# Kernel optimization log

Hardware: AMD Instinct MI355X
Metric: run time of the kernel (lower is better)

Reference implementation:

```python
import jax, jax.numpy as jnp
import numpy as np

N = 50000   # nodes
E = 800000  # directed edges (self loops added in reference)
F = 8       # temporal features
D = 64      # hidden_channels
H = 4       # heads
C = D // H  # per-head channels = 16
L = 3       # num GAT layers
T = 3       # node types
TE = 16     # type embed dim


def _glorot(key, shape):
    fan_in, fan_out = shape[-2], shape[-1]
    s = jnp.sqrt(6.0 / (fan_in + fan_out))
    return jax.random.uniform(key, shape, jnp.float32, -s, s)


def setup_inputs() -> dict:
    key = jax.random.key(0)
    ks = jax.random.split(key, 24)
    return {
        'x': jax.random.normal(ks[0], (N, F), jnp.float32),
        'node_type': jax.random.randint(ks[1], (N,), 0, T),
        'edge_src': jax.random.randint(ks[2], (E,), 0, N),
        'edge_dst': jax.random.randint(ks[3], (E,), 0, N),
        # TemporalEncoder (Linear F->D + ReLU)
        'Wt': _glorot(ks[4], (F, D)), 'bt': jnp.zeros((D,), jnp.float32),
        # type embedding and input projection
        'Et': 0.1 * jax.random.normal(ks[5], (T, TE), jnp.float32),
        'Wp': _glorot(ks[6], (D + TE, D)), 'bp': jnp.zeros((D,), jnp.float32),
        # GATv2 layers (stacked over L)
        'Wl': _glorot(ks[7], (L, D, H * C)), 'bl': jnp.zeros((L, H * C), jnp.float32),
        'Wr': _glorot(ks[8], (L, D, H * C)), 'br': jnp.zeros((L, H * C), jnp.float32),
        'att': _glorot(ks[9], (L, H, C)),
        'Wres': _glorot(ks[10], (L, D, H * C)),
        'bconv': jnp.zeros((L, H * C), jnp.float32),
        'gamma': jnp.ones((L, D), jnp.float32), 'beta': jnp.zeros((L, D), jnp.float32),
        'alpha': jnp.float32(0.5),
        # output head
        'W1': _glorot(ks[11], (D, D // 2)), 'b1': jnp.zeros((D // 2,), jnp.float32),
        'W2': _glorot(ks[12], (D // 2, 1)), 'b2': jnp.zeros((1,), jnp.float32),
    }


def _layernorm(x, g, b, eps=1e-5):
    mu = jnp.mean(x, -1, keepdims=True)
    v = jnp.mean((x - mu) ** 2, -1, keepdims=True)
    return g * (x - mu) / jnp.sqrt(v + eps) + b


def reference(x, node_type, edge_src, edge_dst, Wt, bt, Et, Wp, bp,
              Wl, bl, Wr, br, att, Wres, bconv, gamma, beta, alpha,
              W1, b1, W2, b2):
    # temporal encoder + type embedding + input projection
    h = jax.nn.relu(x @ Wt + bt)                       # [N, D]
    h = jnp.concatenate([h, Et[node_type]], axis=-1) @ Wp + bp
    h0 = h

    # add self loops once (eval mode -> no dropout)
    loop = jnp.arange(N)
    src = jnp.concatenate([edge_src, loop])            # [E']
    dst = jnp.concatenate([edge_dst, loop])

    for l in range(L):
        xl = (h @ Wl[l] + bl[l]).reshape(N, H, C)      # source transform
        xr = (h @ Wr[l] + br[l]).reshape(N, H, C)      # target transform
        e = jax.nn.leaky_relu(xl[src] + xr[dst], 0.2)  # [E', H, C]
        score = jnp.einsum('ehc,hc->eh', e, att[l])    # [E', H]
        # segment softmax over incoming edges of each destination node
        m = jax.ops.segment_max(score, dst, num_segments=N)
        ex = jnp.exp(score - m[dst])
        s = jax.ops.segment_sum(ex, dst, num_segments=N)
        a = ex / (s[dst] + 1e-16)                      # [E', H]
        msg = xl[src] * a[:, :, None]                  # [E', H, C]
        out = jax.ops.segment_sum(msg, dst, num_segments=N).reshape(N, H * C)
        out = out + h @ Wres[l] + bconv[l]             # GATv2 residual + bias
        h = _layernorm(alpha * out + (1.0 - alpha) * h0, gamma[l], beta[l])

    z = jax.nn.relu(h @ W1 + b1)
    return jax.nn.sigmoid(z @ W2 + b2)                 # [N, 1]
```

## Files before the change

### kernel.cpp

```cpp
#include <hip/hip_runtime.h>
#include <hip/hip_bf16.h>

typedef __hip_bfloat16 bf16;
typedef __attribute__((ext_vector_type(8))) short short8;
typedef __attribute__((ext_vector_type(4))) float f32x4;

__device__ __forceinline__ float b2f(bf16 v) { return __bfloat162float(v); }
__device__ __forceinline__ bf16 f2b(float v) { return __float2bfloat16(v); }
__device__ __forceinline__ short f2bs(float v) {
    bf16 b = f2b(v);
    return *reinterpret_cast<short*>(&b);
}
__device__ __forceinline__ float bflo(unsigned int u) { return __uint_as_float(u << 16); }
__device__ __forceinline__ float bfhi(unsigned int u) { return __uint_as_float(u & 0xffff0000u); }
__device__ __forceinline__ unsigned int packbf(float lo, float hi) {
    bf16 l = f2b(lo), h = f2b(hi);
    return ((unsigned int)(*(unsigned short*)&h) << 16) | (*(unsigned short*)&l);
}


__global__ void k_sentinel(float* out, int n, float val) {
    int i = blockIdx.x * blockDim.x + threadIdx.x;
    if (i < n) out[i] = val;
}

#define PREP_BLOCKS 169
__global__ void k_setup(const float* __restrict__ Wl, const float* __restrict__ Wr,
                        const float* __restrict__ Wres, const float* __restrict__ Wp,
                        const float* __restrict__ W1, const float* __restrict__ Et,
                        const float* __restrict__ bp,
                        bf16* __restrict__ WT, bf16* __restrict__ WpT,
                        bf16* __restrict__ W1T, float* __restrict__ TyB,
                        const int* __restrict__ edst, int* __restrict__ counts,
                        int* __restrict__ rank, int e) {
    int b = blockIdx.x;
    if (b < PREP_BLOCKS) {
        int i = b * 256 + threadIdx.x;
        if (i < 36864) {
            int l = i / 12288, rem = i % 12288;
            int col = rem / 64, k = rem % 64;
            int mat = col >> 6, c = col & 63;
            const float* W = (mat == 0) ? Wl : (mat == 1) ? Wr : Wres;
            WT[i] = f2b(W[l * 4096 + k * 64 + c]);
        } else if (i < 40960) {
            int j = i - 36864, col = j / 64, k = j % 64;
            WpT[j] = f2b(Wp[k * 64 + col]);
        } else if (i < 43008) {
            int j = i - 40960, col = j / 64, k = j % 64;
            W1T[j] = f2b(W1[k * 32 + col]);
        } else if (i < 43200) {
            int j = i - 43008, t = j / 64, d = j % 64;
            float s = bp[d];
#pragma unroll
            for (int f = 0; f < 16; ++f) s += Et[t * 16 + f] * Wp[(64 + f) * 64 + d];
            TyB[j] = s;
        }
    } else {
        int i = (b - PREP_BLOCKS) * 256 + threadIdx.x;
        if (i < e) rank[i] = atomicAdd(&counts[edst[i]], 1);
    }
}

__global__ __launch_bounds__(256) void k_encx(
        const float* __restrict__ x, const int* __restrict__ ntype,
        const float* __restrict__ Wt, const float* __restrict__ bt,
        const bf16* __restrict__ WpT, const float* __restrict__ TyB,
        bf16* __restrict__ h0b,
        const bf16* __restrict__ WT0, const float* __restrict__ bl0,
        const float* __restrict__ br0, const float* __restrict__ bc0,
        bf16* __restrict__ xlo, bf16* __restrict__ xro, bf16* __restrict__ reso,
        int n) {
    __shared__ float sWt[512];
    __shared__ float sbt[64];
    __shared__ __align__(16) short sh[4 * 16 * 72];
    int tid = threadIdx.x;
    for (int i = tid; i < 512; i += 256) sWt[i] = Wt[i];
    if (tid < 64) sbt[tid] = bt[tid];
    __syncthreads();
    int wave = tid >> 6, lane = tid & 63;
    int nb = blockIdx.x * 64 + wave * 16;
    if (nb >= n) return;
    int m = lane & 15, q = lane >> 4;
    short* shw = sh + wave * 16 * 72;

    const float* xrow = x + (size_t)(nb + m) * 8;
    float xv[8];
#pragma unroll
    for (int f = 0; f < 8; ++f) xv[f] = xrow[f];

    short8 a0, a1;
#pragma unroll
    for (int j = 0; j < 8; ++j) {
        int c0 = q * 8 + j, c1 = 32 + q * 8 + j;
        float s0 = sbt[c0], s1 = sbt[c1];
#pragma unroll
        for (int f = 0; f < 8; ++f) {
            s0 += xv[f] * sWt[f * 64 + c0];
            s1 += xv[f] * sWt[f * 64 + c1];
        }
        a0[j] = f2bs(fmaxf(s0, 0.f));
        a1[j] = f2bs(fmaxf(s1, 0.f));
    }

    int ty[4];
#pragma unroll
    for (int r = 0; r < 4; ++r) ty[r] = ntype[nb + q * 4 + r];

#pragma unroll
    for (int t = 0; t < 4; ++t) {
        const short* wp = (const short*)(WpT + (size_t)(t * 16 + m) * 64) + q * 8;
        short8 b0 = *(const short8*)(wp);
        short8 b1 = *(const short8*)(wp + 32);
        f32x4 acc = {0.f, 0.f, 0.f, 0.f};
        acc = __builtin_amdgcn_mfma_f32_16x16x32_bf16(a0, b0, acc, 0, 0, 0);
        acc = __builtin_amdgcn_mfma_f32_16x16x32_bf16(a1, b1, acc, 0, 0, 0);
        int col = t * 16 + m;
#pragma unroll
        for (int r = 0; r < 4; ++r) {
            int nd = nb + q * 4 + r;
            short vb = f2bs(acc[r] + TyB[ty[r] * 64 + col]);
            h0b[(size_t)nd * 64 + col] = *reinterpret_cast<bf16*>(&vb);
            shw[(q * 4 + r) * 72 + col] = vb;
        }
    }
    short8 ha0 = *(const short8*)(&shw[m * 72 + q * 8]);
    short8 ha1 = *(const short8*)(&shw[m * 72 + 32 + q * 8]);
#pragma unroll
    for (int t = 0; t < 12; ++t) {
        const short* wp = (const short*)(WT0 + (size_t)(t * 16 + m) * 64) + q * 8;
        short8 b0 = *(const short8*)(wp);
        short8 b1 = *(const short8*)(wp + 32);
        f32x4 acc = {0.f, 0.f, 0.f, 0.f};
        acc = __builtin_amdgcn_mfma_f32_16x16x32_bf16(ha0, b0, acc, 0, 0, 0);
        acc = __builtin_amdgcn_mfma_f32_16x16x32_bf16(ha1, b1, acc, 0, 0, 0);
        int col = t * 16 + m;
        int mat = col >> 6, c = col & 63;
        float bias = (mat == 0) ? bl0[c] : (mat == 1) ? br0[c] : bc0[c];
        bf16* dst = (mat == 0) ? xlo : (mat == 1) ? xro : reso;
#pragma unroll
        for (int r = 0; r < 4; ++r)
            dst[(size_t)(nb + q * 4 + r) * 64 + c] = f2b(acc[r] + bias);
    }
}

__global__ void k_scan_local(const int* __restrict__ counts, int* __restrict__ row_raw,
                             int* __restrict__ bsum, int n) {
    __shared__ int part[256];
    int tid = threadIdx.x;
    int base = blockIdx.x * 1024 + tid * 4;
    int c0 = (base     < n) ? counts[base]     + 1 : 0;
    int c1 = (base + 1 < n) ? counts[base + 1] + 1 : 0;
    int c2 = (base + 2 < n) ? counts[base + 2] + 1 : 0;
    int c3 = (base + 3 < n) ? counts[base + 3] + 1 : 0;
    part[tid] = c0 + c1 + c2 + c3;
    __syncthreads();
    for (int off = 1; off < 256; off <<= 1) {
        int t = (tid >= off) ? part[tid - off] : 0;
        __syncthreads();
        part[tid] += t;
        __syncthreads();
    }
    int ex = (tid == 0) ? 0 : part[tid - 1];
    if (base     < n) row_raw[base]     = ex;
    if (base + 1 < n) row_raw[base + 1] = ex + c0;
    if (base + 2 < n) row_raw[base + 2] = ex + c0 + c1;
    if (base + 3 < n) row_raw[base + 3] = ex + c0 + c1 + c2;
    if (tid == 255) bsum[blockIdx.x] = part[255];
}

__global__ void k_scan_bsum(int* __restrict__ bsum, int* __restrict__ row_ptr,
                            int g, int n) {
    int lane = threadIdx.x;
    int orig = (lane < g) ? bsum[lane] : 0;
    int v = orig;
#pragma unroll
    for (int off = 1; off < 64; off <<= 1) {
        int t = __shfl_up(v, off, 64);
        if (lane >= off) v += t;
    }
    if (lane < g) bsum[lane] = v - orig;
    if (lane == 63) row_ptr[n] = v;
}

__global__ void k_build(const int* __restrict__ src, const int* __restrict__ dst,
                        const int* __restrict__ row_raw, const int* __restrict__ bsum,
                        const int* __restrict__ rank,
                        int* __restrict__ row_ptr, int* __restrict__ csr_src,
                        int n, int e) {
    int i = blockIdx.x * 256 + threadIdx.x;
    if (i < n) {
        int rp = row_raw[i] + bsum[i >> 10];
        row_ptr[i] = rp;
        csr_src[rp] = i;
    }
    if (i < e) {
        int d = dst[i];
        int pos = row_raw[d] + bsum[d >> 10] + 1 + rank[i];
        csr_src[pos] = src[i];
    }
}

#define GAT2_STEP(E_IDX, LS, A0S, A1S)                                            \
    {                                                                             \
        int s_ = csr_src[E_IDX];                                                  \
        unsigned int xu_ = *(const unsigned int*)((const unsigned short*)xl +     \
                                                  (size_t)s_ * 64 + ch);          \
        float x0_ = bflo(xu_), x1_ = bfhi(xu_);                                   \
        float t0_ = x0_ + xr0; t0_ = fmaxf(t0_, 0.2f * t0_);                      \
        float t1_ = x1_ + xr1; t1_ = fmaxf(t1_, 0.2f * t1_);                      \
        float p_ = t0_ * at0 + t1_ * at1;                                         \
        p_ += __shfl_xor(p_, 1, 64);                                              \
        p_ += __shfl_xor(p_, 2, 64);                                              \
        p_ += __shfl_xor(p_, 4, 64);                                              \
        float pe_ = __expf(fminf(p_, 60.f));                                      \
        A0S += pe_ * x0_;  A1S += pe_ * x1_;  LS += pe_;                          \
    }

#define GAT_PHASE_BODY                                                            \
    int tid = threadIdx.x;                                                        \
    int wave = tid >> 6, lane = tid & 63;                                         \
    int half = lane >> 5;                                                         \
    int L = lane & 31;                                                            \
    int head = L >> 3, cp = L & 7;                                                \
    int ch = head * 16 + cp * 2;                                                  \
    int nl = wave * 2 + half;                                                     \
    int v = blockIdx.x * 16 + nl;                                                 \
    bool valid = v < n;                                                           \
    int vv = valid ? v : 0;                                                       \
    unsigned int xru = *(const unsigned int*)((const unsigned short*)xr +         \
                                              (size_t)vv * 64 + ch);              \
    float xr0 = bflo(xru), xr1 = bfhi(xru);                                       \
    float at0 = att[ch], at1 = att[ch + 1];                                       \
    int beg = row_ptr[vv];                                                        \
    int end = valid ? row_ptr[vv + 1] : beg;                                      \
    float l0 = 0.f, A00 = 0.f, A01 = 0.f;                                         \
    float l1 = 0.f, A10 = 0.f, A11 = 0.f;                                         \
    float l2 = 0.f, A20 = 0.f, A21 = 0.f;                                         \
    float l3 = 0.f, A30 = 0.f, A31 = 0.f;                                         \
    int e = beg;                                                                  \
    for (; e + 3 < end; e += 4) {                                                 \
        GAT2_STEP(e,     l0, A00, A01)                                            \
        GAT2_STEP(e + 1, l1, A10, A11)                                            \
        GAT2_STEP(e + 2, l2, A20, A21)                                            \
        GAT2_STEP(e + 3, l3, A30, A31)                                            \
    }                                                                             \
    int rem = end - e;                                                            \
    if (rem > 0) GAT2_STEP(e,     l0, A00, A01)                                   \
    if (rem > 1) GAT2_STEP(e + 1, l1, A10, A11)                                   \
    if (rem > 2) GAT2_STEP(e + 2, l2, A20, A21)                                   \
    float lsum = (l0 + l1) + (l2 + l3);                                           \
    float inv = 1.f / (lsum + 1e-16f);                                            \
    float acc0 = ((A00 + A10) + (A20 + A30)) * inv;                               \
    float acc1 = ((A01 + A11) + (A21 + A31)) * inv;                               \
    unsigned int ru = *(const unsigned int*)((const unsigned short*)res +         \
                                             (size_t)vv * 64 + ch);               \
    unsigned int hu = *(const unsigned int*)((const unsigned short*)h0b +         \
                                             (size_t)vv * 64 + ch);               \
    float o0 = acc0 + bflo(ru);                                                   \
    float o1 = acc1 + bfhi(ru);                                                   \
    float a = alpha_p[0];                                                         \
    float t0 = a * o0 + (1.f - a) * bflo(hu);                                     \
    float t1 = a * o1 + (1.f - a) * bfhi(hu);                                     \
    float mu = t0 + t1;                                                           \
    _Pragma("unroll")                                                             \
    for (int o = 1; o < 32; o <<= 1) mu += __shfl_xor(mu, o, 64);                 \
    mu *= (1.f / 64.f);                                                           \
    float d0 = t0 - mu, d1 = t1 - mu;                                             \
    float var = d0 * d0 + d1 * d1;                                                \
    _Pragma("unroll")                                                             \
    for (int o = 1; o < 32; o <<= 1) var += __shfl_xor(var, o, 64);               \
    var *= (1.f / 64.f);                                                          \
    float rs = rsqrtf(var + 1e-5f);                                               \
    float hn0 = gamma[ch] * d0 * rs + beta[ch];                                   \
    float hn1 = gamma[ch + 1] * d1 * rs + beta[ch + 1];                           \
    *(unsigned int*)((char*)sh + nl * 144 + ch * 2) = packbf(hn0, hn1);           \
    __syncthreads();

__global__ __launch_bounds__(512) void k_gatx(
        const bf16* __restrict__ xl, const bf16* __restrict__ xr,
        const bf16* __restrict__ res, const bf16* __restrict__ h0b,
        const float* __restrict__ att, const float* __restrict__ gamma,
        const float* __restrict__ beta, const float* __restrict__ alpha_p,
        const int* __restrict__ row_ptr, const int* __restrict__ csr_src,
        const bf16* __restrict__ WTn, const float* __restrict__ bln,
        const float* __restrict__ brn, const float* __restrict__ bcn,
        bf16* __restrict__ xlo, bf16* __restrict__ xro, bf16* __restrict__ reso,
        int n) {
    __shared__ __align__(16) short sh[16 * 72];
    GAT_PHASE_BODY

    int m = lane & 15, q = lane >> 4;
    short8 ha0 = *(const short8*)(&sh[m * 72 + q * 8]);
    short8 ha1 = *(const short8*)(&sh[m * 72 + 32 + q * 8]);
    int nb = blockIdx.x * 16;
    for (int t = wave; t < 12; t += 8) {
        const short* wp = (const short*)(WTn + (size_t)(t * 16 + m) * 64) + q * 8;
        short8 b0 = *(const short8*)(wp);
        short8 b1 = *(const short8*)(wp + 32);
        f32x4 acc = {0.f, 0.f, 0.f, 0.f};
        acc = __builtin_amdgcn_mfma_f32_16x16x32_bf16(ha0, b0, acc, 0, 0, 0);
        acc = __builtin_amdgcn_mfma_f32_16x16x32_bf16(ha1, b1, acc, 0, 0, 0);
        int col = t * 16 + m;
        int mat = col >> 6, c = col & 63;
        float bias = (mat == 0) ? bln[c] : (mat == 1) ? brn[c] : bcn[c];
        bf16* dst = (mat == 0) ? xlo : (mat == 1) ? xro : reso;
#pragma unroll
        for (int r = 0; r < 4; ++r) {
            int nd = nb + q * 4 + r;
            if (nd < n) dst[(size_t)nd * 64 + c] = f2b(acc[r] + bias);
        }
    }
}

__global__ __launch_bounds__(512) void k_gath(
        const bf16* __restrict__ xl, const bf16* __restrict__ xr,
        const bf16* __restrict__ res, const bf16* __restrict__ h0b,
        const float* __restrict__ att, const float* __restrict__ gamma,
        const float* __restrict__ beta, const float* __restrict__ alpha_p,
        const int* __restrict__ row_ptr, const int* __restrict__ csr_src,
        const bf16* __restrict__ W1T, const float* __restrict__ b1,
        const float* __restrict__ W2, const float* __restrict__ b2,
        float* __restrict__ out, int n) {
    __shared__ __align__(16) short sh[16 * 72];
    GAT_PHASE_BODY

    if (wave == 0) {
        int m = lane & 15, q = lane >> 4;
        short8 ha0 = *(const short8*)(&sh[m * 72 + q * 8]);
        short8 ha1 = *(const short8*)(&sh[m * 72 + 32 + q * 8]);

        const short* w0p = (const short*)(W1T + (size_t)m * 64) + q * 8;
        const short* w1p = (const short*)(W1T + (size_t)(16 + m) * 64) + q * 8;
        short8 b00 = *(const short8*)(w0p);
        short8 b01 = *(const short8*)(w0p + 32);
        short8 b10 = *(const short8*)(w1p);
        short8 b11 = *(const short8*)(w1p + 32);

        f32x4 acc0 = {0.f, 0.f, 0.f, 0.f};
        f32x4 acc1 = {0.f, 0.f, 0.f, 0.f};
        acc0 = __builtin_amdgcn_mfma_f32_16x16x32_bf16(ha0, b00, acc0, 0, 0, 0);
        acc0 = __builtin_amdgcn_mfma_f32_16x16x32_bf16(ha1, b01, acc0, 0, 0, 0);
        acc1 = __builtin_amdgcn_mfma_f32_16x16x32_bf16(ha0, b10, acc1, 0, 0, 0);
        acc1 = __builtin_amdgcn_mfma_f32_16x16x32_bf16(ha1, b11, acc1, 0, 0, 0);

        float w2a = W2[m], w2b = W2[16 + m];
        float bb0 = b1[m], bb1 = b1[16 + m];
        float part[4];
#pragma unroll
        for (int r = 0; r < 4; ++r)
            part[r] = fmaxf(acc0[r] + bb0, 0.f) * w2a + fmaxf(acc1[r] + bb1, 0.f) * w2b;
#pragma unroll
        for (int mask = 1; mask < 16; mask <<= 1) {
#pragma unroll
            for (int r = 0; r < 4; ++r) part[r] += __shfl_xor(part[r], mask, 64);
        }
        if (m == 0) {
            float bb2 = b2[0];
            int nb = blockIdx.x * 16;
#pragma unroll
            for (int r = 0; r < 4; ++r) {
                int nd = nb + q * 4 + r;
                if (nd < n) out[nd] = 1.f / (1.f + __expf(-(part[r] + bb2)));
            }
        }
    }
}

extern "C" void kernel_launch(void* const* d_in, const int* in_sizes, int n_in,
                              void* d_out, int out_size, void* d_ws, size_t ws_size,
                              hipStream_t stream) {
    const float* x     = (const float*)d_in[0];
    const int*   ntype = (const int*)d_in[1];
    const int*   esrc  = (const int*)d_in[2];
    const int*   edst  = (const int*)d_in[3];
    const float* Wt    = (const float*)d_in[4];
    const float* bt    = (const float*)d_in[5];
    const float* Et    = (const float*)d_in[6];
    const float* Wp    = (const float*)d_in[7];
    const float* bp    = (const float*)d_in[8];
    const float* Wl    = (const float*)d_in[9];
    const float* bl    = (const float*)d_in[10];
    const float* Wr    = (const float*)d_in[11];
    const float* br    = (const float*)d_in[12];
    const float* att   = (const float*)d_in[13];
    const float* Wres  = (const float*)d_in[14];
    const float* bconv = (const float*)d_in[15];
    const float* gamma = (const float*)d_in[16];
    const float* beta  = (const float*)d_in[17];
    const float* alpha = (const float*)d_in[18];
    const float* W1    = (const float*)d_in[19];
    const float* b1    = (const float*)d_in[20];
    const float* W2    = (const float*)d_in[21];
    const float* b2    = (const float*)d_in[22];
    float* out = (float*)d_out;

    const int N = in_sizes[1];
    const int E = in_sizes[2];

    const int G = (N + 1023) / 1024;

    size_t need = 256
                + (size_t)N * 64 * 2 * 7
                + (size_t)36864 * 2 + (size_t)4096 * 2 + (size_t)2048 * 2
                + (size_t)192 * 4
                + (size_t)N * 4
                + (size_t)(N + 1) * 4
                + (size_t)N * 4
                + (size_t)E * 4
                + 256
                + (size_t)(E + N) * 4;

    if (ws_size < need) {
        k_sentinel<<<(N + 255) / 256, 256, 0, stream>>>(out, N,
                                                        100.0f + (float)(ws_size >> 20));
        return;
    }

    char* ws = (char*)d_ws;
    ws += 256;
    bf16* h0b   = (bf16*)ws;  ws += (size_t)N * 64 * 2;
    bf16* xlA   = (bf16*)ws;  ws += (size_t)N * 64 * 2;
    bf16* xrA   = (bf16*)ws;  ws += (size_t)N * 64 * 2;
    bf16* resA  = (bf16*)ws;  ws += (size_t)N * 64 * 2;
    bf16* xlB   = (bf16*)ws;  ws += (size_t)N * 64 * 2;
    bf16* xrB   = (bf16*)ws;  ws += (size_t)N * 64 * 2;
    bf16* resB  = (bf16*)ws;  ws += (size_t)N * 64 * 2;
    bf16* WT    = (bf16*)ws;  ws += (size_t)36864 * 2;
    bf16* WpT   = (bf16*)ws;  ws += (size_t)4096 * 2;
    bf16* W1T   = (bf16*)ws;  ws += (size_t)2048 * 2;
    float* TyB  = (float*)ws; ws += (size_t)192 * 4;
    int* row_raw = (int*)ws;  ws += (size_t)N * 4;
    int* row_ptr = (int*)ws;  ws += (size_t)(N + 1) * 4;
    int* counts  = (int*)ws;  ws += (size_t)N * 4;
    int* rank    = (int*)ws;  ws += (size_t)E * 4;
    int* bsum    = (int*)ws;  ws += 256;
    int* csr_src = (int*)ws;  ws += (size_t)(E + N) * 4;

    hipMemsetAsync(counts, 0, (size_t)N * 4, stream);
    k_setup<<<PREP_BLOCKS + (E + 255) / 256, 256, 0, stream>>>(
        Wl, Wr, Wres, Wp, W1, Et, bp, WT, WpT, W1T, TyB, edst, counts, rank, E);
    k_encx<<<(N + 63) / 64, 256, 0, stream>>>(x, ntype, Wt, bt, WpT, TyB, h0b,
                                              WT, bl, br, bconv, xlA, xrA, resA, N);
    k_scan_local<<<G, 256, 0, stream>>>(counts, row_raw, bsum, N);
    k_scan_bsum<<<1, 64, 0, stream>>>(bsum, row_ptr, G, N);
    k_build<<<(E + 255) / 256, 256, 0, stream>>>(esrc, edst, row_raw, bsum, rank,
                                                 row_ptr, csr_src, N, E);

    k_gatx<<<(N + 15) / 16, 512, 0, stream>>>(
        xlA, xrA, resA, h0b, att, gamma, beta, alpha, row_ptr, csr_src,
        WT + 12288, bl + 64, br + 64, bconv + 64, xlB, xrB, resB, N);
    k_gatx<<<(N + 15) / 16, 512, 0, stream>>>(
        xlB, xrB, resB, h0b, att + 64, gamma + 64, beta + 64, alpha, row_ptr, csr_src,
        WT + 24576, bl + 128, br + 128, bconv + 128, xlA, xrA, resA, N);
    k_gath<<<(N + 15) / 16, 512, 0, stream>>>(
        xlA, xrA, resA, h0b, att + 128, gamma + 128, beta + 128, alpha,
        row_ptr, csr_src, W1T, b1, W2, b2, out, N);
}
```

Measured before the change: 321.2 us.

## Sort nodes by in-degree bucket so GAT blocks process similar-degree nodes

Builds a degree histogram during the scan, then a counting-sort permutation of nodes by in-degree (capped at 63). The GAT kernels take their nodes through this permutation, so the half-waves and blocks that share work have similar edge counts, which cuts divergence and tail imbalance. The cost is an extra histogram, atomics, a permutation array, and scattered writes of outputs by node id that lose the coalescing of sequential nodes.

```diff
diff --git a/kernel.cpp b/kernel.cpp
--- a/kernel.cpp
+++ b/kernel.cpp
@@ -144,14 +144,22 @@
 }
 
 __global__ void k_scan_local(const int* __restrict__ counts, int* __restrict__ row_raw,
-                             int* __restrict__ bsum, int n) {
+                             int* __restrict__ bsum, int* __restrict__ hist, int n) {
     __shared__ int part[256];
+    __shared__ int lh[64];
     int tid = threadIdx.x;
+    if (tid < 64) lh[tid] = 0;
+    __syncthreads();
     int base = blockIdx.x * 1024 + tid * 4;
-    int c0 = (base     < n) ? counts[base]     + 1 : 0;
-    int c1 = (base + 1 < n) ? counts[base + 1] + 1 : 0;
-    int c2 = (base + 2 < n) ? counts[base + 2] + 1 : 0;
-    int c3 = (base + 3 < n) ? counts[base + 3] + 1 : 0;
+    int d0 = (base     < n) ? counts[base]     : -1;
+    int d1 = (base + 1 < n) ? counts[base + 1] : -1;
+    int d2 = (base + 2 < n) ? counts[base + 2] : -1;
+    int d3 = (base + 3 < n) ? counts[base + 3] : -1;
+    if (d0 >= 0) atomicAdd(&lh[d0 < 63 ? d0 : 63], 1);
+    if (d1 >= 0) atomicAdd(&lh[d1 < 63 ? d1 : 63], 1);
+    if (d2 >= 0) atomicAdd(&lh[d2 < 63 ? d2 : 63], 1);
+    if (d3 >= 0) atomicAdd(&lh[d3 < 63 ? d3 : 63], 1);
+    int c0 = d0 + 1, c1 = d1 + 1, c2 = d2 + 1, c3 = d3 + 1;
     part[tid] = c0 + c1 + c2 + c3;
     __syncthreads();
     for (int off = 1; off < 256; off <<= 1) {
@@ -166,10 +174,11 @@
     if (base + 2 < n) row_raw[base + 2] = ex + c0 + c1;
     if (base + 3 < n) row_raw[base + 3] = ex + c0 + c1 + c2;
     if (tid == 255) bsum[blockIdx.x] = part[255];
+    if (tid < 64 && lh[tid] > 0) atomicAdd(&hist[tid], lh[tid]);
 }
 
 __global__ void k_scan_bsum(int* __restrict__ bsum, int* __restrict__ row_ptr,
-                            int g, int n) {
+                            int* __restrict__ hist, int g, int n) {
     int lane = threadIdx.x;
     int orig = (lane < g) ? bsum[lane] : 0;
     int v = orig;
@@ -180,14 +189,42 @@
     }
     if (lane < g) bsum[lane] = v - orig;
     if (lane == 63) row_ptr[n] = v;
+
+    int ho = hist[lane];
+    int hv = ho;
+#pragma unroll
+    for (int off = 1; off < 64; off <<= 1) {
+        int t = __shfl_up(hv, off, 64);
+        if (lane >= off) hv += t;
+    }
+    hist[lane] = hv - ho;
 }
 
 __global__ void k_build(const int* __restrict__ src, const int* __restrict__ dst,
                         const int* __restrict__ row_raw, const int* __restrict__ bsum,
-                        const int* __restrict__ rank,
+                        const int* __restrict__ rank, const int* __restrict__ counts,
                         int* __restrict__ row_ptr, int* __restrict__ csr_src,
+                        int* __restrict__ hist, int* __restrict__ perm,
                         int n, int e) {
-    int i = blockIdx.x * 256 + threadIdx.x;
+    __shared__ int lh[64];
+    __shared__ int gbase[64];
+    int tid = threadIdx.x;
+    int i = blockIdx.x * 256 + tid;
+    bool nodework = (blockIdx.x * 256) < n;
+    if (nodework) {
+        if (tid < 64) lh[tid] = 0;
+        __syncthreads();
+        int bucket = 0, myrank = -1;
+        if (i < n) {
+            int d = counts[i];
+            bucket = d < 63 ? d : 63;
+            myrank = atomicAdd(&lh[bucket], 1);
+        }
+        __syncthreads();
+        if (tid < 64 && lh[tid] > 0) gbase[tid] = atomicAdd(&hist[tid], lh[tid]);
+        __syncthreads();
+        if (i < n) perm[gbase[bucket] + myrank] = i;
+    }
     if (i < n) {
         int rp = row_raw[i] + bsum[i >> 10];
         row_ptr[i] = rp;
@@ -224,15 +261,16 @@
     int head = L >> 3, cp = L & 7;                                                \
     int ch = head * 16 + cp * 2;                                                  \
     int nl = wave * 2 + half;                                                     \
-    int v = blockIdx.x * 16 + nl;                                                 \
-    bool valid = v < n;                                                           \
-    int vv = valid ? v : 0;                                                       \
+    int idx = blockIdx.x * 16 + nl;                                               \
+    bool valid = idx < n;                                                         \
+    int v = valid ? perm[idx] : 0;                                                \
+    if (L == 0) sid[nl] = valid ? v : -1;                                         \
     unsigned int xru = *(const unsigned int*)((const unsigned short*)xr +         \
-                                              (size_t)vv * 64 + ch);              \
+                                              (size_t)v * 64 + ch);               \
     float xr0 = bflo(xru), xr1 = bfhi(xru);                                       \
     float at0 = att[ch], at1 = att[ch + 1];                                       \
-    int beg = row_ptr[vv];                                                        \
-    int end = valid ? row_ptr[vv + 1] : beg;                                      \
+    int beg = row_ptr[v];                                                         \
+    int end = valid ? row_ptr[v + 1] : beg;                                       \
     float l0 = 0.f, A00 = 0.f, A01 = 0.f;                                         \
     float l1 = 0.f, A10 = 0.f, A11 = 0.f;                                         \
     float l2 = 0.f, A20 = 0.f, A21 = 0.f;                                         \
@@ -253,9 +291,9 @@
     float acc0 = ((A00 + A10) + (A20 + A30)) * inv;                               \
     float acc1 = ((A01 + A11) + (A21 + A31)) * inv;                               \
     unsigned int ru = *(const unsigned int*)((const unsigned short*)res +         \
-                                             (size_t)vv * 64 + ch);               \
+                                             (size_t)v * 64 + ch);                \
     unsigned int hu = *(const unsigned int*)((const unsigned short*)h0b +         \
-                                             (size_t)vv * 64 + ch);               \
+                                             (size_t)v * 64 + ch);                \
     float o0 = acc0 + bflo(ru);                                                   \
     float o1 = acc1 + bfhi(ru);                                                   \
     float a = alpha_p[0];                                                         \
@@ -282,17 +320,18 @@
         const float* __restrict__ att, const float* __restrict__ gamma,
         const float* __restrict__ beta, const float* __restrict__ alpha_p,
         const int* __restrict__ row_ptr, const int* __restrict__ csr_src,
+        const int* __restrict__ perm,
         const bf16* __restrict__ WTn, const float* __restrict__ bln,
         const float* __restrict__ brn, const float* __restrict__ bcn,
         bf16* __restrict__ xlo, bf16* __restrict__ xro, bf16* __restrict__ reso,
         int n) {
     __shared__ __align__(16) short sh[16 * 72];
+    __shared__ int sid[16];
     GAT_PHASE_BODY
 
     int m = lane & 15, q = lane >> 4;
     short8 ha0 = *(const short8*)(&sh[m * 72 + q * 8]);
     short8 ha1 = *(const short8*)(&sh[m * 72 + 32 + q * 8]);
-    int nb = blockIdx.x * 16;
     for (int t = wave; t < 12; t += 8) {
         const short* wp = (const short*)(WTn + (size_t)(t * 16 + m) * 64) + q * 8;
         short8 b0 = *(const short8*)(wp);
@@ -306,8 +345,8 @@
         bf16* dst = (mat == 0) ? xlo : (mat == 1) ? xro : reso;
 #pragma unroll
         for (int r = 0; r < 4; ++r) {
-            int nd = nb + q * 4 + r;
-            if (nd < n) dst[(size_t)nd * 64 + c] = f2b(acc[r] + bias);
+            int nd = sid[q * 4 + r];
+            if (nd >= 0) dst[(size_t)nd * 64 + c] = f2b(acc[r] + bias);
         }
     }
 }
@@ -318,10 +357,12 @@
         const float* __restrict__ att, const float* __restrict__ gamma,
         const float* __restrict__ beta, const float* __restrict__ alpha_p,
         const int* __restrict__ row_ptr, const int* __restrict__ csr_src,
+        const int* __restrict__ perm,
         const bf16* __restrict__ W1T, const float* __restrict__ b1,
         const float* __restrict__ W2, const float* __restrict__ b2,
         float* __restrict__ out, int n) {
     __shared__ __align__(16) short sh[16 * 72];
+    __shared__ int sid[16];
     GAT_PHASE_BODY
 
     if (wave == 0) {
@@ -356,11 +397,10 @@
         }
         if (m == 0) {
             float bb2 = b2[0];
-            int nb = blockIdx.x * 16;
 #pragma unroll
             for (int r = 0; r < 4; ++r) {
-                int nd = nb + q * 4 + r;
-                if (nd < n) out[nd] = 1.f / (1.f + __expf(-(part[r] + bb2)));
+                int nd = sid[q * 4 + r];
+                if (nd >= 0) out[nd] = 1.f / (1.f + __expf(-(part[r] + bb2)));
             }
         }
     }
@@ -405,6 +445,7 @@
                 + (size_t)192 * 4
                 + (size_t)N * 4
                 + (size_t)(N + 1) * 4
+                + (size_t)(N + 64) * 4
                 + (size_t)N * 4
                 + (size_t)E * 4
                 + 256
@@ -432,27 +473,30 @@
     int* row_raw = (int*)ws;  ws += (size_t)N * 4;
     int* row_ptr = (int*)ws;  ws += (size_t)(N + 1) * 4;
     int* counts  = (int*)ws;  ws += (size_t)N * 4;
+    int* hist    = (int*)ws;  ws += (size_t)64 * 4;
+    int* perm    = (int*)ws;  ws += (size_t)N * 4;
     int* rank    = (int*)ws;  ws += (size_t)E * 4;
     int* bsum    = (int*)ws;  ws += 256;
     int* csr_src = (int*)ws;  ws += (size_t)(E + N) * 4;
 
-    hipMemsetAsync(counts, 0, (size_t)N * 4, stream);
+    hipMemsetAsync(counts, 0, (size_t)(N + 64) * 4, stream);
     k_setup<<<PREP_BLOCKS + (E + 255) / 256, 256, 0, stream>>>(
         Wl, Wr, Wres, Wp, W1, Et, bp, WT, WpT, W1T, TyB, edst, counts, rank, E);
     k_encx<<<(N + 63) / 64, 256, 0, stream>>>(x, ntype, Wt, bt, WpT, TyB, h0b,
                                               WT, bl, br, bconv, xlA, xrA, resA, N);
-    k_scan_local<<<G, 256, 0, stream>>>(counts, row_raw, bsum, N);
-    k_scan_bsum<<<1, 64, 0, stream>>>(bsum, row_ptr, G, N);
+    k_scan_local<<<G, 256, 0, stream>>>(counts, row_raw, bsum, hist, N);
+    k_scan_bsum<<<1, 64, 0, stream>>>(bsum, row_ptr, hist, G, N);
     k_build<<<(E + 255) / 256, 256, 0, stream>>>(esrc, edst, row_raw, bsum, rank,
-                                                 row_ptr, csr_src, N, E);
+                                                 counts, row_ptr, csr_src, hist, perm,
+                                                 N, E);
 
     k_gatx<<<(N + 15) / 16, 512, 0, stream>>>(
-        xlA, xrA, resA, h0b, att, gamma, beta, alpha, row_ptr, csr_src,
+        xlA, xrA, resA, h0b, att, gamma, beta, alpha, row_ptr, csr_src, perm,
         WT + 12288, bl + 64, br + 64, bconv + 64, xlB, xrB, resB, N);
     k_gatx<<<(N + 15) / 16, 512, 0, stream>>>(
         xlB, xrB, resB, h0b, att + 64, gamma + 64, beta + 64, alpha, row_ptr, csr_src,
-        WT + 24576, bl + 128, br + 128, bconv + 128, xlA, xrA, resA, N);
+        perm, WT + 24576, bl + 128, br + 128, bconv + 128, xlA, xrA, resA, N);
     k_gath<<<(N + 15) / 16, 512, 0, stream>>>(
         xlA, xrA, resA, h0b, att + 128, gamma + 128, beta + 128, alpha,
-        row_ptr, csr_src, W1T, b1, W2, b2, out, N);
-}
+        row_ptr, csr_src, perm, W1T, b1, W2, b2, out, N);
+}
```

Measured after the change: 315.0 us (median of 2 runs). Within noise of the previous version (-1.9%).
